# Kernel tuning notes

Hardware: AMD Instinct MI355X
Metric: run time of the kernel (lower is better)

## Reference

```python
import jax, jax.numpy as jnp
import numpy as np
from jax import lax

N = 16384
K = 16
EPS = 1e-5


def setup_inputs() -> dict:
    key = jax.random.key(0)
    ks = jax.random.split(key, 10)

    def w(k, shape):
        fan_in = shape[0]
        return jax.random.normal(k, shape, jnp.float32) / np.sqrt(fan_in)

    return {
        "pos": jax.random.normal(ks[0], (N, 3), jnp.float32),
        "normal": jax.random.normal(ks[1], (N, 3), jnp.float32),
        # conv1 mlp: Linear(9,64) -> GroupNorm(8,64) -> ReLU -> Linear(64,64)
        "W1a": w(ks[2], (9, 64)), "b1a": jnp.zeros((64,), jnp.float32),
        "g1": jnp.ones((64,), jnp.float32), "beta1": jnp.zeros((64,), jnp.float32),
        "W1b": w(ks[3], (64, 64)), "b1b": jnp.zeros((64,), jnp.float32),
        # conv2 mlp: Linear(67,64) -> GroupNorm(8,64) -> ReLU -> Linear(64,64)
        "W2a": w(ks[4], (67, 64)), "b2a": jnp.zeros((64,), jnp.float32),
        "g2": jnp.ones((64,), jnp.float32), "beta2": jnp.zeros((64,), jnp.float32),
        "W2b": w(ks[5], (64, 64)), "b2b": jnp.zeros((64,), jnp.float32),
        # conv3 mlp: Linear(67,128) -> GroupNorm(16,128) -> ReLU -> Linear(128,128)
        "W3a": w(ks[6], (67, 128)), "b3a": jnp.zeros((128,), jnp.float32),
        "g3": jnp.ones((128,), jnp.float32), "beta3": jnp.zeros((128,), jnp.float32),
        "W3b": w(ks[7], (128, 128)), "b3b": jnp.zeros((128,), jnp.float32),
    }


def knn_graph(pos, k):
    # [N,N] squared distances; loop=True -> self is included (distance 0).
    sq = jnp.sum(pos * pos, axis=1)
    d2 = sq[:, None] + sq[None, :] - 2.0 * (pos @ pos.T)
    _, nbr = lax.top_k(-d2, k)  # [N,k] neighbor (source) indices per target node
    return nbr


def group_norm(h, gamma, beta, groups):
    # h: [N,k,C]; normalize each group of channels per edge sample.
    n, k, c = h.shape
    hg = h.reshape(n, k, groups, c // groups)
    mu = hg.mean(axis=-1, keepdims=True)
    var = hg.var(axis=-1, keepdims=True)
    hg = (hg - mu) * lax.rsqrt(var + EPS)
    return hg.reshape(n, k, c) * gamma + beta


def pointnet_conv(x, pos, nbr, Wa, ba, gamma, beta, Wb, bb, groups):
    # message: concat(x_j, pos_j - pos_i), MLP per edge, max-aggregate over neighbors
    xj = x[nbr]                              # [N,k,C_in]
    rel = pos[nbr] - pos[:, None, :]         # [N,k,3]
    m = jnp.concatenate([xj, rel], axis=-1)  # [N,k,C_in+3]
    h = m @ Wa + ba
    h = jax.nn.relu(group_norm(h, gamma, beta, groups))
    h = h @ Wb + bb
    return jnp.max(h, axis=1)                # [N,C_out]


def reference(pos, normal, W1a, b1a, g1, beta1, W1b, b1b,
              W2a, b2a, g2, beta2, W2b, b2b,
              W3a, b3a, g3, beta3, W3b, b3b):
    nbr = knn_graph(pos, K)
    h = jnp.concatenate([pos, normal], axis=-1)  # [N,6]
    h1 = jax.nn.relu(pointnet_conv(h, pos, nbr, W1a, b1a, g1, beta1, W1b, b1b, 8))
    h2 = jax.nn.relu(pointnet_conv(h1, pos, nbr, W2a, b2a, g2, beta2, W2b, b2b, 8))
    h3 = jax.nn.relu(pointnet_conv(h2, pos, nbr, W3a, b3a, g3, beta3, W3b, b3b, 16))
    return (h1, h2, h3)
```

## Files before the change

### kernel.cpp

```cpp
#include <hip/hip_runtime.h>
#include <hip/hip_bf16.h>
#include <stdint.h>

typedef unsigned long long u64;
typedef unsigned int u32;
typedef __attribute__((ext_vector_type(8))) short bf16x8;
typedef __attribute__((ext_vector_type(8))) unsigned short u16x8;
typedef __attribute__((ext_vector_type(4))) float f32x4;

__device__ __forceinline__ float ldv(const void* p, size_t idx, int mode) {
  return mode ? __bfloat162float(((const __hip_bfloat16*)p)[idx])
              : ((const float*)p)[idx];
}
__device__ __forceinline__ void stv(void* p, size_t idx, int mode, float v) {
  if (mode) ((__hip_bfloat16*)p)[idx] = __float2bfloat16(v);
  else      ((float*)p)[idx] = v;
}
__device__ __forceinline__ unsigned short f2bfb(float f) {
  u32 u = __float_as_uint(f);
  u32 r = u + 0x7fffu + ((u >> 16) & 1u);
  return (unsigned short)(r >> 16);
}
__device__ __forceinline__ float bfb2f(unsigned short b) {
  return __uint_as_float((u32)b << 16);
}
__device__ __forceinline__ u64 shfl64(u64 v, int src) {
  int lo = __shfl((int)(u32)(v & 0xffffffffu), src, 64);
  int hi = __shfl((int)(u32)(v >> 32), src, 64);
  return ((u64)(u32)hi << 32) | (u32)lo;
}
__device__ __forceinline__ u64 shflxor64(u64 v, int m) {
  int lo = __shfl_xor((int)(u32)(v & 0xffffffffu), m, 64);
  int hi = __shfl_xor((int)(u32)(v >> 32), m, 64);
  return ((u64)(u32)hi << 32) | (u32)lo;
}
__device__ __forceinline__ u64 shfl64w16(u64 v, int src) {
  int lo = __shfl((int)(u32)(v & 0xffffffffu), src, 16);
  int hi = __shfl((int)(u32)(v >> 32), src, 16);
  return ((u64)(u32)hi << 32) | (u32)lo;
}

__device__ __forceinline__ u32 benc(float f) {
  u32 u = __float_as_uint(f);
  return (u & 0x80000000u) ? ~u : (u | 0x80000000u);
}
__device__ __forceinline__ float bdec(u32 k) {
  return (k & 0x80000000u) ? __uint_as_float(k ^ 0x80000000u)
                           : __uint_as_float(~k);
}

__global__ void PointNetSimple_61409442398998_kernel() {}

struct CvtEnt { const void* src; float* dst; int n; };
struct CvtArgs { CvtEnt e[12]; };
struct WEnt { const void* src; unsigned short* dst; int K, N, Kpad; };
struct WArgs { WEnt e[6]; };

__global__ void setup_kernel(const void* __restrict__ pos,
                             const void* __restrict__ nrm,
                             WArgs wa, CvtArgs ca,
                             int* __restrict__ flag,
                             float4* __restrict__ pos4,
                             float* __restrict__ h0, int n) {
  const unsigned short* u16p = (const unsigned short*)pos;
  int cnt = 0;
  for (int k = 0; k < 32; ++k) {
    int e = (u16p[k] >> 7) & 0xff;
    if (e >= 110 && e <= 140) cnt++;
  }
  const int mode = (cnt >= 26) ? 1 : 0;

  const int nprep = n >> 8;
  const int b = blockIdx.x;
  if (b < nprep) {
    int i = b * 256 + threadIdx.x;
    float x = ldv(pos, 3*(size_t)i+0, mode);
    float y = ldv(pos, 3*(size_t)i+1, mode);
    float z = ldv(pos, 3*(size_t)i+2, mode);
    pos4[i] = make_float4(x, y, z, x*x + y*y + z*z);
    h0[6*(size_t)i+0] = x; h0[6*(size_t)i+1] = y; h0[6*(size_t)i+2] = z;
    h0[6*(size_t)i+3] = ldv(nrm, 3*(size_t)i+0, mode);
    h0[6*(size_t)i+4] = ldv(nrm, 3*(size_t)i+1, mode);
    h0[6*(size_t)i+5] = ldv(nrm, 3*(size_t)i+2, mode);
    float bmn[3] = {x, y, z}, bmx[3] = {x, y, z};
#pragma unroll
    for (int m = 32; m; m >>= 1) {
#pragma unroll
      for (int k = 0; k < 3; ++k) {
        bmn[k] = fminf(bmn[k], __shfl_xor(bmn[k], m, 64));
        bmx[k] = fmaxf(bmx[k], __shfl_xor(bmx[k], m, 64));
      }
    }
    if ((threadIdx.x & 63) == 0) {
      u32* bb = (u32*)flag;
#pragma unroll
      for (int k = 0; k < 3; ++k) {
        atomicMin(&bb[4 + k], benc(bmn[k]));
        atomicMax(&bb[7 + k], benc(bmx[k]));
      }
    }
  } else {
    int r = b - nprep;
    if (r < 6) {
      WEnt ent = wa.e[r];
      for (int t = threadIdx.x; t < ent.N * ent.Kpad; t += blockDim.x) {
        int nn = t / ent.Kpad;
        int k  = t - nn * ent.Kpad;
        float v = (k < ent.K) ? ldv(ent.src, (size_t)k * ent.N + nn, mode) : 0.0f;
        ent.dst[t] = f2bfb(v);
      }
      if (r == 0 && threadIdx.x == 0) flag[0] = mode;
    } else {
      for (int t2 = 0; t2 < 12; ++t2) {
        CvtEnt ent = ca.e[t2];
        for (int t = threadIdx.x; t < ent.n; t += blockDim.x)
          ent.dst[t] = ldv(ent.src, t, mode);
      }
    }
  }
}

template<int CAP>
__device__ __forceinline__ void knn_flush(u64* __restrict__ wbuf, int& cnt,
                                          u64& val, u64& t15, float& th,
                                          int lane) {
  u64 cand = (lane < cnt) ? wbuf[lane] : ~0ull;
#pragma unroll
  for (int k = 2; k <= CAP; k <<= 1) {
#pragma unroll
    for (int j = k >> 1; j > 0; j >>= 1) {
      u64 other = shflxor64(cand, j);
      bool up    = ((lane & k) == 0) || (k == CAP);
      bool lower = ((lane & j) == 0);
      bool keepMin = (up == lower);
      u64 mn = cand < other ? cand : other;
      u64 mx = cand < other ? other : cand;
      cand = keepMin ? mn : mx;
    }
  }
  u64 rev = shfl64w16(cand, 15 - (lane & 15));
  u64 lo = val < rev ? val : rev;
#pragma unroll
  for (int j = 8; j > 0; j >>= 1) {
    u64 other = shflxor64(lo, j);
    bool lower = ((lane & j) == 0);
    u64 mn = lo < other ? lo : other;
    u64 mx = lo < other ? other : lo;
    lo = lower ? mn : mx;
  }
  val = (lane < 16) ? lo : ~0ull;
  t15 = shfl64(val, 15);
  u32 thb = (u32)(t15 >> 32);
  th = (thb == 0xffffffffu) ? 3.4e38f : __uint_as_float(thb);
  cnt = 0;
}

#define GR 32
#define GR3 (GR*GR*GR)

__global__ __launch_bounds__(256) void hist_kernel(
    const float4* __restrict__ pos4, const u32* __restrict__ bbx,
    int* __restrict__ counts, int* __restrict__ cid, int n) {
  const int i = blockIdx.x * 256 + threadIdx.x;
  if (i >= n) return;
  const float mnx = bdec(bbx[0]), mny = bdec(bbx[1]), mnz = bdec(bbx[2]);
  const float ihx = (float)GR / fmaxf(bdec(bbx[3]) - mnx, 1e-20f);
  const float ihy = (float)GR / fmaxf(bdec(bbx[4]) - mny, 1e-20f);
  const float ihz = (float)GR / fmaxf(bdec(bbx[5]) - mnz, 1e-20f);
  float4 p = pos4[i];
  int cx = min(GR - 1, max(0, (int)((p.x - mnx) * ihx)));
  int cy = min(GR - 1, max(0, (int)((p.y - mny) * ihy)));
  int cz = min(GR - 1, max(0, (int)((p.z - mnz) * ihz)));
  int lin = (cz * GR + cy) * GR + cx;
  cid[i] = lin;
  atomicAdd(&counts[lin], 1);
}

__global__ __launch_bounds__(1024) void scan_kernel(
    const int* __restrict__ counts, int* __restrict__ cellstart,
    int* __restrict__ cursor) {
  __shared__ int part[1024];
  const int t = threadIdx.x;
  const int base = t * 32;
  int v[32];
  int s = 0;
#pragma unroll
  for (int k = 0; k < 32; ++k) { v[k] = counts[base + k]; s += v[k]; }
  part[t] = s;
  __syncthreads();
  for (int d = 1; d < 1024; d <<= 1) {
    int x = (t >= d) ? part[t - d] : 0;
    __syncthreads();
    part[t] += x;
    __syncthreads();
  }
  int off = part[t] - s;
#pragma unroll
  for (int k = 0; k < 32; ++k) {
    cellstart[base + k] = off; cursor[base + k] = off; off += v[k];
  }
  if (t == 1023) { cellstart[GR3] = off; cursor[GR3] = off; }
}

__global__ __launch_bounds__(256) void scatter_kernel(
    const float4* __restrict__ pos4, const int* __restrict__ cid,
    int* __restrict__ cursor, int* __restrict__ sidx,
    float4* __restrict__ spos4, int n) {
  const int i = blockIdx.x * 256 + threadIdx.x;
  if (i >= n) return;
  int dst = atomicAdd(&cursor[cid[i]], 1);
  spos4[dst] = pos4[i];
  sidx[dst]  = i;
}

#define KNN7_WPB 4
__global__ __launch_bounds__(256) void knn7_kernel(
    const float4* __restrict__ spos4,
    const int* __restrict__ sidx, const int* __restrict__ cellstart,
    const u32* __restrict__ bbx, int* __restrict__ nbr, int n) {
  __shared__ u64 buf[KNN7_WPB][72];
  const int tid = threadIdx.x, lane = tid & 63, w = tid >> 6;
  const int g = blockIdx.x * KNN7_WPB + w;
  u64* wbuf = &buf[w][0];
  const float4 pi = spos4[g];
  const int target = sidx[g];

  const float mnx = bdec(bbx[0]), mny = bdec(bbx[1]), mnz = bdec(bbx[2]);
  const float ex = fmaxf(bdec(bbx[3]) - mnx, 1e-20f);
  const float ey = fmaxf(bdec(bbx[4]) - mny, 1e-20f);
  const float ez = fmaxf(bdec(bbx[5]) - mnz, 1e-20f);
  const float ihx = (float)GR / ex, ihy = (float)GR / ey, ihz = (float)GR / ez;
  const float hxf = ex * (1.0f / GR), hyf = ey * (1.0f / GR), hzf = ez * (1.0f / GR);
  const int cx = min(GR - 1, max(0, (int)((pi.x - mnx) * ihx)));
  const int cy = min(GR - 1, max(0, (int)((pi.y - mny) * ihy)));
  const int cz = min(GR - 1, max(0, (int)((pi.z - mnz) * ihz)));

  u64 val = ~0ull, t15 = ~0ull;
  float th = 3.4e38f;
  int cnt = 0;
  int myseen = 0;

  auto doFlush = [&]() {
    if (cnt <= 32) knn_flush<32>(wbuf, cnt, val, t15, th, lane);
    else           knn_flush<64>(wbuf, cnt, val, t15, th, lane);
  };

  auto procSeg = [&](int p0, int p1) {
#pragma unroll 2
    for (int t0 = p0; t0 < p1; t0 += 64) {
      int gi = t0 + lane;
      bool in = gi < p1;
      float4 a = spos4[in ? gi : (p1 - 1)];
      float d2 = (pi.w + a.w) - 2.0f*(pi.x*a.x + pi.y*a.y + pi.z*a.z);
      d2 = fmaxf(d2, 0.0f);
      bool pass = in && (d2 <= th);
      u64 bal = __ballot(pass);
      if (bal) {
        int pc = __popcll(bal);
        if (cnt + pc > 64) doFlush();
        u32 mb = __builtin_amdgcn_mbcnt_lo((u32)bal, 0u);
        mb = __builtin_amdgcn_mbcnt_hi((u32)(bal >> 32), mb);
        if (pass)
          wbuf[cnt + mb] = ((u64)__float_as_uint(d2) << 32) | (u32)sidx[gi];
        cnt += pc;
      }
    }
  };

  {
    const int oc = (cz * GR + cy) * GR + cx;
    const int oLo = cellstart[oc], oHi = cellstart[oc + 1];
    if (lane == 0) myseen += oHi - oLo;
    procSeg(oLo, oHi);
    if (cnt > 0) doFlush();
  }

  for (int r = 1; r < GR; ++r) {
    const int x0 = max(cx - r, 0), x1 = min(cx + r, GR - 1);
    const int d1 = 2*r + 1, d2i = 2*r - 1;
    const int nA = 2 * d1;
    const int nB = 2 * d2i;
    const int nC = 2 * d2i * d2i;
    const int S = nA + nB + nC;
    const u32 magic = 0xFFFFFFFFu / (u32)d2i + 1u;

    for (int b0 = 0; b0 < S; b0 += 64) {
      const int s = b0 + lane;
      int zc = 0, yc = 0, xa = 0, xb = -1;
      bool live = s < S;
      if (live) {
        if (s < nA) {
          int za = s >= d1;
          int dy = s - (za ? d1 : 0) - r;
          zc = cz + (za ? r : -r); yc = cy + dy; xa = x0; xb = x1;
        } else if (s < nA + nB) {
          int t = s - nA;
          int side = t >= d2i;
          int dz = t - (side ? d2i : 0) - (r - 1);
          zc = cz + dz; yc = cy + (side ? r : -r); xa = x0; xb = x1;
        } else {
          int t = s - nA - nB;
          int side = t & 1; t >>= 1;
          int dzi = (int)__umulhi((u32)t, magic);
          int dyi = t - dzi * d2i;
          zc = cz - r + 1 + dzi; yc = cy - r + 1 + dyi;
          int xcell = side ? cx + r : cx - r;
          xa = xcell; xb = xcell;
          live = ((unsigned)xcell < GR);
        }
        live = live && ((unsigned)zc < GR) && ((unsigned)yc < GR);
      }
      int lo = 0, hi = 0;
      if (live) {
        int base = (zc * GR + yc) * GR;
        lo = cellstart[base + xa];
        hi = cellstart[base + xb + 1];
        myseen += hi - lo;
      }
      u64 bal = __ballot(live && (hi > lo));
      while (bal) {
        int l = __builtin_ctzll(bal); bal &= bal - 1;
        int p0 = __shfl(lo, l, 64), p1 = __shfl(hi, l, 64);
        procSeg(p0, p1);
      }
    }

    int tot = myseen;
#pragma unroll
    for (int m = 32; m; m >>= 1) tot += __shfl_xor(tot, m, 64);
    if (tot >= n) break;
    float mind = 3.4e38f;
    if (cx - r > 0)      mind = fminf(mind, pi.x - (mnx + (float)(cx - r) * hxf));
    if (cx + r < GR - 1) mind = fminf(mind, (mnx + (float)(cx + r + 1) * hxf) - pi.x);
    if (cy - r > 0)      mind = fminf(mind, pi.y - (mny + (float)(cy - r) * hyf));
    if (cy + r < GR - 1) mind = fminf(mind, (mny + (float)(cy + r + 1) * hyf) - pi.y);
    if (cz - r > 0)      mind = fminf(mind, pi.z - (mnz + (float)(cz - r) * hzf));
    if (cz + r < GR - 1) mind = fminf(mind, (mnz + (float)(cz + r + 1) * hzf) - pi.z);
    float mind2 = mind * mind * 0.9999f - 1e-6f;
    if (mind2 > th) break;
    if (cnt > 0) {
      doFlush();
      if (mind2 > th) break;
    }
  }
  if (cnt > 0) doFlush();
  if (lane < 16) nbr[(size_t)target * 16 + lane] = (int)(val & 0xffffffffu);
}

template<int CIN, int CMID, int KT1, int NT, int KT2>
__global__ __launch_bounds__(256, 4) void conv_mfma7_kernel(
    const float* __restrict__ xf,
    const unsigned short* __restrict__ xb,
    const float4* __restrict__ pos4,
    const int* __restrict__ nbr,
    const int* __restrict__ flag,
    const unsigned short* __restrict__ WaT,
    const unsigned short* __restrict__ WbT,
    const float* __restrict__ baf,
    const float* __restrict__ gmf,
    const float* __restrict__ btf,
    const float* __restrict__ bbf,
    unsigned short* __restrict__ xoutb,
    void* __restrict__ bout, size_t out_off)
{
  constexpr int K1PAD = KT1 * 32;
  constexpr int SB = CMID + 8;

  __shared__ unsigned short msgB[128 * SB];

  const int tid  = threadIdx.x;
  const int lane = tid & 63;
  const int w    = tid >> 6;
  const int quad = lane >> 4;
  const int cl   = lane & 15;
  const int node0 = blockIdx.x * 8;
  const int mode = flag[0];

  bf16x8 afr[2][KT1];
#pragma unroll
  for (int mt = 0; mt < 2; ++mt) {
    const int node = node0 + w*2 + mt;
    const int j = nbr[(size_t)node*16 + cl];
    const float4 pin = pos4[node];
    const float4 pj = pos4[j];
    const float rx = pj.x - pin.x, ry = pj.y - pin.y, rz = pj.z - pin.z;
    if constexpr (CIN == 64) {
#pragma unroll
      for (int kt = 0; kt < 2; ++kt)
        afr[mt][kt] = *(const bf16x8*)&xb[(size_t)j*64 + kt*32 + quad*8];
      unsigned short o[8] = {0,0,0,0,0,0,0,0};
      if (quad == 0) { o[0] = f2bfb(rx); o[1] = f2bfb(ry); o[2] = f2bfb(rz); }
      afr[mt][KT1-1] = *(bf16x8*)o;
    } else {
      unsigned short o[8] = {0,0,0,0,0,0,0,0};
      if (quad == 0) {
        const float* p = &xf[(size_t)j*6];
        o[0] = f2bfb(p[0]); o[1] = f2bfb(p[1]); o[2] = f2bfb(p[2]);
        o[3] = f2bfb(p[3]); o[4] = f2bfb(p[4]); o[5] = f2bfb(p[5]);
        o[6] = f2bfb(rx);   o[7] = f2bfb(ry);
      } else if (quad == 1) {
        o[0] = f2bfb(rz);
      }
      afr[mt][0] = *(bf16x8*)o;
    }
  }

  const int grow = lane >> 1, ggl = lane & 1;
  bf16x8 w1c[KT1], w1n[KT1];
#pragma unroll
  for (int kt = 0; kt < KT1; ++kt)
    w1c[kt] = *(const bf16x8*)&WaT[(size_t)cl * K1PAD + kt*32 + quad*8];
#pragma unroll
  for (int nt = 0; nt < NT; ++nt) {
    if (nt + 1 < NT) {
#pragma unroll
      for (int kt = 0; kt < KT1; ++kt)
        w1n[kt] = *(const bf16x8*)&WaT[(size_t)((nt+1)*16 + cl) * K1PAD + kt*32 + quad*8];
    }
    f32x4 a1[2];
    a1[0] = (f32x4){0.f, 0.f, 0.f, 0.f};
    a1[1] = (f32x4){0.f, 0.f, 0.f, 0.f};
#pragma unroll
    for (int kt = 0; kt < KT1; ++kt) {
      a1[0] = __builtin_amdgcn_mfma_f32_16x16x32_bf16(afr[0][kt], w1c[kt], a1[0], 0, 0, 0);
      a1[1] = __builtin_amdgcn_mfma_f32_16x16x32_bf16(afr[1][kt], w1c[kt], a1[1], 0, 0, 0);
    }
    float bac = baf[nt*16 + cl];
#pragma unroll
    for (int mt = 0; mt < 2; ++mt)
#pragma unroll
      for (int reg = 0; reg < 4; ++reg)
        msgB[(w*32 + mt*16 + quad*4 + reg) * SB + nt*16 + cl] =
            f2bfb(a1[mt][reg] + bac);
    asm volatile("" ::: "memory");
    {
      const int cb = nt*16 + ggl*8;
      unsigned short* p = &msgB[(w*32 + grow) * SB + cb];
      u16x8 hv = *(const u16x8*)p;
      float vv[8];
#pragma unroll
      for (int e = 0; e < 8; ++e) vv[e] = bfb2f(hv[e]);
      float s = 0.f, q = 0.f;
#pragma unroll
      for (int e = 0; e < 8; ++e) { s += vv[e]; q += vv[e]*vv[e]; }
      float mu = s * 0.125f;
      float var = q * 0.125f - mu * mu;
      float inv = rsqrtf(fmaxf(var, 0.0f) + 1e-5f);
      unsigned short o[8];
#pragma unroll
      for (int e = 0; e < 8; ++e) {
        float t = (vv[e] - mu) * inv * gmf[cb+e] + btf[cb+e];
        o[e] = f2bfb(fmaxf(t, 0.0f));
      }
      *(bf16x8*)p = *(bf16x8*)o;
    }
    asm volatile("" ::: "memory");
#pragma unroll
    for (int kt = 0; kt < KT1; ++kt) w1c[kt] = w1n[kt];
  }

  bf16x8 af0[KT2], af1[KT2];
#pragma unroll
  for (int kt = 0; kt < KT2; ++kt) {
    af0[kt] = *(const bf16x8*)&msgB[(w*32 + cl)      * SB + kt*32 + quad*8];
    af1[kt] = *(const bf16x8*)&msgB[(w*32 + 16 + cl) * SB + kt*32 + quad*8];
  }
  bf16x8 w2c[KT2], w2n[KT2];
#pragma unroll
  for (int kt = 0; kt < KT2; ++kt)
    w2c[kt] = *(const bf16x8*)&WbT[(size_t)cl * CMID + kt*32 + quad*8];
#pragma unroll
  for (int nt = 0; nt < NT; ++nt) {
    if (nt + 1 < NT) {
#pragma unroll
      for (int kt = 0; kt < KT2; ++kt)
        w2n[kt] = *(const bf16x8*)&WbT[(size_t)((nt+1)*16 + cl) * CMID + kt*32 + quad*8];
    }
    f32x4 a2[2];
    a2[0] = (f32x4){0.f, 0.f, 0.f, 0.f};
    a2[1] = (f32x4){0.f, 0.f, 0.f, 0.f};
#pragma unroll
    for (int kt = 0; kt < KT2; ++kt) {
      a2[0] = __builtin_amdgcn_mfma_f32_16x16x32_bf16(af0[kt], w2c[kt], a2[0], 0, 0, 0);
      a2[1] = __builtin_amdgcn_mfma_f32_16x16x32_bf16(af1[kt], w2c[kt], a2[1], 0, 0, 0);
    }
#pragma unroll
    for (int mt = 0; mt < 2; ++mt) {
      int node = node0 + w*2 + mt;
      float m = fmaxf(fmaxf(a2[mt][0], a2[mt][1]),
                      fmaxf(a2[mt][2], a2[mt][3]));
      m = fmaxf(m, __shfl_xor(m, 16, 64));
      m = fmaxf(m, __shfl_xor(m, 32, 64));
      float v = fmaxf(m + bbf[nt*16 + cl], 0.0f);
      if (quad == 0) {
        size_t oi = (size_t)node * CMID + nt*16 + cl;
        if (xoutb) xoutb[oi] = f2bfb(v);
        stv(bout, out_off + oi, mode, v);
      }
    }
#pragma unroll
    for (int kt = 0; kt < KT2; ++kt) w2c[kt] = w2n[kt];
  }
}

extern "C" void kernel_launch(void* const* d_in, const int* in_sizes, int n_in,
                              void* d_out, int out_size, void* d_ws, size_t ws_size,
                              hipStream_t stream) {
  (void)n_in; (void)ws_size; (void)in_sizes;
  int n = out_size / 256;
  if (n <= 0 || (n & 255)) n = 16384;

  float* ws = (float*)d_ws;
  int*    flag    = (int*)ws;
  float4* pos4    = (float4*)(ws + 16);
  float*  h0      = ws + 16 + (size_t)4*n;
  int*    nbr     = (int*)(ws + 16 + (size_t)10*n);
  unsigned short* h1b = (unsigned short*)(ws + 16 + (size_t)26*n);
  unsigned short* h2b = (unsigned short*)(ws + 16 + (size_t)58*n);
  float*  vbuf    = ws + 16 + (size_t)90*n;
  unsigned short* wtbuf = (unsigned short*)(vbuf + 1024);

  float* gbase = vbuf + 1024 + 22528;
  int*    cid       = (int*)gbase;
  int*    counts    = cid + n;
  int*    cellstart = counts + GR3;
  int*    cursor    = cellstart + 32772;
  int*    sidx      = cursor + 32772;
  float4* spos4     = (float4*)(sidx + n);

  const int vsz[12] = {64,64,64,64, 64,64,64,64, 128,128,128,128};
  const int vsrc[12] = {3,4,5,7, 9,10,11,13, 15,16,17,19};
  CvtArgs ca;
  float* vptr[12];
  {
    int off = 0;
    for (int t = 0; t < 12; ++t) {
      ca.e[t].src = d_in[vsrc[t]];
      ca.e[t].dst = vbuf + off;
      ca.e[t].n   = vsz[t];
      vptr[t] = vbuf + off;
      off += vsz[t];
    }
  }
  const int wK[6]    = {9, 64, 67, 64, 67, 128};
  const int wN[6]    = {64, 64, 64, 64, 128, 128};
  const int wKp[6]   = {32, 64, 96, 64, 96, 128};
  const int wsrc[6]  = {2, 6, 8, 12, 14, 18};
  WArgs wa;
  unsigned short* wptr[6];
  {
    int off = 0;
    for (int t = 0; t < 6; ++t) {
      wa.e[t].src  = d_in[wsrc[t]];
      wa.e[t].dst  = wtbuf + off;
      wa.e[t].K    = wK[t];
      wa.e[t].N    = wN[t];
      wa.e[t].Kpad = wKp[t];
      wptr[t] = wtbuf + off;
      off += wN[t] * wKp[t];
    }
  }

  u32* bbx = (u32*)ws + 4;
  hipMemsetAsync(bbx,     0xFF, 12, stream);
  hipMemsetAsync(bbx + 3, 0x00, 12, stream);
  hipMemsetAsync(counts,  0x00, GR3 * sizeof(int), stream);

  setup_kernel<<<n/256 + 7, 256, 0, stream>>>(
      d_in[0], d_in[1], wa, ca, flag, pos4, h0, n);

  hist_kernel<<<n/256, 256, 0, stream>>>(pos4, bbx, counts, cid, n);
  scan_kernel<<<1, 1024, 0, stream>>>(counts, cellstart, cursor);
  scatter_kernel<<<n/256, 256, 0, stream>>>(pos4, cid, cursor, sidx, spos4, n);
  knn7_kernel<<<n/KNN7_WPB, 256, 0, stream>>>(spos4, sidx, cellstart,
                                              bbx, nbr, n);

  conv_mfma7_kernel<6, 64, 1, 4, 2><<<n/8, 256, 0, stream>>>(
      h0, (const unsigned short*)nullptr, pos4, nbr, flag, wptr[0], wptr[1],
      vptr[0], vptr[1], vptr[2], vptr[3], h1b, d_out, (size_t)0);
  conv_mfma7_kernel<64, 64, 3, 4, 2><<<n/8, 256, 0, stream>>>(
      (const float*)nullptr, h1b, pos4, nbr, flag, wptr[2], wptr[3],
      vptr[4], vptr[5], vptr[6], vptr[7], h2b, d_out, (size_t)n*64);
  conv_mfma7_kernel<64, 128, 3, 8, 4><<<n/8, 256, 0, stream>>>(
      (const float*)nullptr, h2b, pos4, nbr, flag, wptr[4], wptr[5],
      vptr[8], vptr[9], vptr[10], vptr[11],
      (unsigned short*)nullptr, d_out, (size_t)n*128);
}
```

Measured before the change: 351.6 us.

## Fold memsets into setup kernel and make kNN a persistent work-stealing kernel

Removes two of the three memsets: the bbox max is now encoded as a negated min, so a single 0xFF memset covers all six words, and the cell-count zeroing moves into extra setup_kernel blocks. The scan kernel now uses int4 vector loads and stores, and resets counts[0] so it can be reused as an atomic work counter. The kNN kernel becomes persistent: 1024 blocks whose wavefronts take query points from that atomic counter, which balances the uneven per-point search cost. This adds an atomic per query and depends on counts[0] being zeroed before the kNN launch.

```diff
diff --git a/kernel.cpp b/kernel.cpp
--- a/kernel.cpp
+++ b/kernel.cpp
@@ -56,12 +56,16 @@
 struct WEnt { const void* src; unsigned short* dst; int K, N, Kpad; };
 struct WArgs { WEnt e[6]; };
 
+#define GR 32
+#define GR3 (GR*GR*GR)
+
 __global__ void setup_kernel(const void* __restrict__ pos,
                              const void* __restrict__ nrm,
                              WArgs wa, CvtArgs ca,
                              int* __restrict__ flag,
                              float4* __restrict__ pos4,
-                             float* __restrict__ h0, int n) {
+                             float* __restrict__ h0,
+                             int* __restrict__ counts, int n) {
   const unsigned short* u16p = (const unsigned short*)pos;
   int cnt = 0;
   for (int k = 0; k < 32; ++k) {
@@ -96,7 +100,7 @@
 #pragma unroll
       for (int k = 0; k < 3; ++k) {
         atomicMin(&bb[4 + k], benc(bmn[k]));
-        atomicMax(&bb[7 + k], benc(bmx[k]));
+        atomicMin(&bb[7 + k], benc(-bmx[k]));
       }
     }
   } else {
@@ -110,12 +114,14 @@
         ent.dst[t] = f2bfb(v);
       }
       if (r == 0 && threadIdx.x == 0) flag[0] = mode;
-    } else {
+    } else if (r == 6) {
       for (int t2 = 0; t2 < 12; ++t2) {
         CvtEnt ent = ca.e[t2];
         for (int t = threadIdx.x; t < ent.n; t += blockDim.x)
           ent.dst[t] = ldv(ent.src, t, mode);
       }
+    } else {
+      counts[(r - 7) * 256 + threadIdx.x] = 0;
     }
   }
 }
@@ -155,18 +161,15 @@
   cnt = 0;
 }
 
-#define GR 32
-#define GR3 (GR*GR*GR)
-
 __global__ __launch_bounds__(256) void hist_kernel(
     const float4* __restrict__ pos4, const u32* __restrict__ bbx,
     int* __restrict__ counts, int* __restrict__ cid, int n) {
   const int i = blockIdx.x * 256 + threadIdx.x;
   if (i >= n) return;
   const float mnx = bdec(bbx[0]), mny = bdec(bbx[1]), mnz = bdec(bbx[2]);
-  const float ihx = (float)GR / fmaxf(bdec(bbx[3]) - mnx, 1e-20f);
-  const float ihy = (float)GR / fmaxf(bdec(bbx[4]) - mny, 1e-20f);
-  const float ihz = (float)GR / fmaxf(bdec(bbx[5]) - mnz, 1e-20f);
+  const float ihx = (float)GR / fmaxf(-bdec(bbx[3]) - mnx, 1e-20f);
+  const float ihy = (float)GR / fmaxf(-bdec(bbx[4]) - mny, 1e-20f);
+  const float ihz = (float)GR / fmaxf(-bdec(bbx[5]) - mnz, 1e-20f);
   float4 p = pos4[i];
   int cx = min(GR - 1, max(0, (int)((p.x - mnx) * ihx)));
   int cy = min(GR - 1, max(0, (int)((p.y - mny) * ihy)));
@@ -181,25 +184,34 @@
     int* __restrict__ cursor) {
   __shared__ int part[1024];
   const int t = threadIdx.x;
-  const int base = t * 32;
-  int v[32];
+  int4 v[8];
   int s = 0;
 #pragma unroll
-  for (int k = 0; k < 32; ++k) { v[k] = counts[base + k]; s += v[k]; }
+  for (int k = 0; k < 8; ++k) {
+    v[k] = ((const int4*)counts)[t*8 + k];
+    s += v[k].x + v[k].y + v[k].z + v[k].w;
+  }
   part[t] = s;
   __syncthreads();
+  if (t == 0) ((int*)counts)[0] = 0;
   for (int d = 1; d < 1024; d <<= 1) {
     int x = (t >= d) ? part[t - d] : 0;
     __syncthreads();
     part[t] += x;
     __syncthreads();
   }
-  int off = part[t] - s;
-#pragma unroll
-  for (int k = 0; k < 32; ++k) {
-    cellstart[base + k] = off; cursor[base + k] = off; off += v[k];
-  }
-  if (t == 1023) { cellstart[GR3] = off; cursor[GR3] = off; }
+  int o = part[t] - s;
+#pragma unroll
+  for (int k = 0; k < 8; ++k) {
+    int4 c;
+    c.x = o; o += v[k].x;
+    c.y = o; o += v[k].y;
+    c.z = o; o += v[k].z;
+    c.w = o; o += v[k].w;
+    ((int4*)cellstart)[t*8 + k] = c;
+    ((int4*)cursor)[t*8 + k] = c;
+  }
+  if (t == 1023) { cellstart[GR3] = o; cursor[GR3] = o; }
 }
 
 __global__ __launch_bounds__(256) void scatter_kernel(
@@ -213,138 +225,146 @@
   sidx[dst]  = i;
 }
 
-#define KNN7_WPB 4
-__global__ __launch_bounds__(256) void knn7_kernel(
+#define KNN_BLOCKS 1024
+__global__ __launch_bounds__(256) void knn7p_kernel(
     const float4* __restrict__ spos4,
     const int* __restrict__ sidx, const int* __restrict__ cellstart,
-    const u32* __restrict__ bbx, int* __restrict__ nbr, int n) {
-  __shared__ u64 buf[KNN7_WPB][72];
+    const u32* __restrict__ bbx, int* __restrict__ nbr,
+    int* __restrict__ ctr, int n) {
+  __shared__ u64 buf[4][72];
   const int tid = threadIdx.x, lane = tid & 63, w = tid >> 6;
-  const int g = blockIdx.x * KNN7_WPB + w;
   u64* wbuf = &buf[w][0];
-  const float4 pi = spos4[g];
-  const int target = sidx[g];
 
   const float mnx = bdec(bbx[0]), mny = bdec(bbx[1]), mnz = bdec(bbx[2]);
-  const float ex = fmaxf(bdec(bbx[3]) - mnx, 1e-20f);
-  const float ey = fmaxf(bdec(bbx[4]) - mny, 1e-20f);
-  const float ez = fmaxf(bdec(bbx[5]) - mnz, 1e-20f);
+  const float ex = fmaxf(-bdec(bbx[3]) - mnx, 1e-20f);
+  const float ey = fmaxf(-bdec(bbx[4]) - mny, 1e-20f);
+  const float ez = fmaxf(-bdec(bbx[5]) - mnz, 1e-20f);
   const float ihx = (float)GR / ex, ihy = (float)GR / ey, ihz = (float)GR / ez;
   const float hxf = ex * (1.0f / GR), hyf = ey * (1.0f / GR), hzf = ez * (1.0f / GR);
-  const int cx = min(GR - 1, max(0, (int)((pi.x - mnx) * ihx)));
-  const int cy = min(GR - 1, max(0, (int)((pi.y - mny) * ihy)));
-  const int cz = min(GR - 1, max(0, (int)((pi.z - mnz) * ihz)));
-
-  u64 val = ~0ull, t15 = ~0ull;
-  float th = 3.4e38f;
-  int cnt = 0;
-  int myseen = 0;
-
-  auto doFlush = [&]() {
-    if (cnt <= 32) knn_flush<32>(wbuf, cnt, val, t15, th, lane);
-    else           knn_flush<64>(wbuf, cnt, val, t15, th, lane);
-  };
-
-  auto procSeg = [&](int p0, int p1) {
+
+  for (;;) {
+    int g0 = 0;
+    if (lane == 0) g0 = atomicAdd(ctr, 1);
+    const int g = __shfl(g0, 0, 64);
+    if (g >= n) break;
+
+    const float4 pi = spos4[g];
+    const int target = sidx[g];
+    const int cx = min(GR - 1, max(0, (int)((pi.x - mnx) * ihx)));
+    const int cy = min(GR - 1, max(0, (int)((pi.y - mny) * ihy)));
+    const int cz = min(GR - 1, max(0, (int)((pi.z - mnz) * ihz)));
+
+    u64 val = ~0ull, t15 = ~0ull;
+    float th = 3.4e38f;
+    int cnt = 0;
+    int myseen = 0;
+
+    auto doFlush = [&]() {
+      if (cnt <= 32) knn_flush<32>(wbuf, cnt, val, t15, th, lane);
+      else           knn_flush<64>(wbuf, cnt, val, t15, th, lane);
+    };
+
+    auto procSeg = [&](int p0, int p1) {
 #pragma unroll 2
-    for (int t0 = p0; t0 < p1; t0 += 64) {
-      int gi = t0 + lane;
-      bool in = gi < p1;
-      float4 a = spos4[in ? gi : (p1 - 1)];
-      float d2 = (pi.w + a.w) - 2.0f*(pi.x*a.x + pi.y*a.y + pi.z*a.z);
-      d2 = fmaxf(d2, 0.0f);
-      bool pass = in && (d2 <= th);
-      u64 bal = __ballot(pass);
-      if (bal) {
-        int pc = __popcll(bal);
-        if (cnt + pc > 64) doFlush();
-        u32 mb = __builtin_amdgcn_mbcnt_lo((u32)bal, 0u);
-        mb = __builtin_amdgcn_mbcnt_hi((u32)(bal >> 32), mb);
-        if (pass)
-          wbuf[cnt + mb] = ((u64)__float_as_uint(d2) << 32) | (u32)sidx[gi];
-        cnt += pc;
-      }
-    }
-  };
-
-  {
-    const int oc = (cz * GR + cy) * GR + cx;
-    const int oLo = cellstart[oc], oHi = cellstart[oc + 1];
-    if (lane == 0) myseen += oHi - oLo;
-    procSeg(oLo, oHi);
+      for (int t0 = p0; t0 < p1; t0 += 64) {
+        int gi = t0 + lane;
+        bool in = gi < p1;
+        float4 a = spos4[in ? gi : (p1 - 1)];
+        float d2 = (pi.w + a.w) - 2.0f*(pi.x*a.x + pi.y*a.y + pi.z*a.z);
+        d2 = fmaxf(d2, 0.0f);
+        bool pass = in && (d2 <= th);
+        u64 bal = __ballot(pass);
+        if (bal) {
+          int pc = __popcll(bal);
+          if (cnt + pc > 64) doFlush();
+          u32 mb = __builtin_amdgcn_mbcnt_lo((u32)bal, 0u);
+          mb = __builtin_amdgcn_mbcnt_hi((u32)(bal >> 32), mb);
+          if (pass)
+            wbuf[cnt + mb] = ((u64)__float_as_uint(d2) << 32) | (u32)sidx[gi];
+          cnt += pc;
+        }
+      }
+    };
+
+    {
+      const int oc = (cz * GR + cy) * GR + cx;
+      const int oLo = cellstart[oc], oHi = cellstart[oc + 1];
+      if (lane == 0) myseen += oHi - oLo;
+      procSeg(oLo, oHi);
+      if (cnt > 0) doFlush();
+    }
+
+    for (int r = 1; r < GR; ++r) {
+      const int x0 = max(cx - r, 0), x1 = min(cx + r, GR - 1);
+      const int d1 = 2*r + 1, d2i = 2*r - 1;
+      const int nA = 2 * d1;
+      const int nB = 2 * d2i;
+      const int nC = 2 * d2i * d2i;
+      const int S = nA + nB + nC;
+      const u32 magic = 0xFFFFFFFFu / (u32)d2i + 1u;
+
+      for (int b0 = 0; b0 < S; b0 += 64) {
+        const int s = b0 + lane;
+        int zc = 0, yc = 0, xa = 0, xb = -1;
+        bool live = s < S;
+        if (live) {
+          if (s < nA) {
+            int za = s >= d1;
+            int dy = s - (za ? d1 : 0) - r;
+            zc = cz + (za ? r : -r); yc = cy + dy; xa = x0; xb = x1;
+          } else if (s < nA + nB) {
+            int t = s - nA;
+            int side = t >= d2i;
+            int dz = t - (side ? d2i : 0) - (r - 1);
+            zc = cz + dz; yc = cy + (side ? r : -r); xa = x0; xb = x1;
+          } else {
+            int t = s - nA - nB;
+            int side = t & 1; t >>= 1;
+            int dzi = (int)__umulhi((u32)t, magic);
+            int dyi = t - dzi * d2i;
+            zc = cz - r + 1 + dzi; yc = cy - r + 1 + dyi;
+            int xcell = side ? cx + r : cx - r;
+            xa = xcell; xb = xcell;
+            live = ((unsigned)xcell < GR);
+          }
+          live = live && ((unsigned)zc < GR) && ((unsigned)yc < GR);
+        }
+        int lo = 0, hi = 0;
+        if (live) {
+          int base = (zc * GR + yc) * GR;
+          lo = cellstart[base + xa];
+          hi = cellstart[base + xb + 1];
+          myseen += hi - lo;
+        }
+        u64 bal = __ballot(live && (hi > lo));
+        while (bal) {
+          int l = __builtin_ctzll(bal); bal &= bal - 1;
+          int p0 = __shfl(lo, l, 64), p1 = __shfl(hi, l, 64);
+          procSeg(p0, p1);
+        }
+      }
+
+      int tot = myseen;
+#pragma unroll
+      for (int m = 32; m; m >>= 1) tot += __shfl_xor(tot, m, 64);
+      if (tot >= n) break;
+      float mind = 3.4e38f;
+      if (cx - r > 0)      mind = fminf(mind, pi.x - (mnx + (float)(cx - r) * hxf));
+      if (cx + r < GR - 1) mind = fminf(mind, (mnx + (float)(cx + r + 1) * hxf) - pi.x);
+      if (cy - r > 0)      mind = fminf(mind, pi.y - (mny + (float)(cy - r) * hyf));
+      if (cy + r < GR - 1) mind = fminf(mind, (mny + (float)(cy + r + 1) * hyf) - pi.y);
+      if (cz - r > 0)      mind = fminf(mind, pi.z - (mnz + (float)(cz - r) * hzf));
+      if (cz + r < GR - 1) mind = fminf(mind, (mnz + (float)(cz + r + 1) * hzf) - pi.z);
+      float mind2 = mind * mind * 0.9999f - 1e-6f;
+      if (mind2 > th) break;
+      if (cnt > 0) {
+        doFlush();
+        if (mind2 > th) break;
+      }
+    }
     if (cnt > 0) doFlush();
-  }
-
-  for (int r = 1; r < GR; ++r) {
-    const int x0 = max(cx - r, 0), x1 = min(cx + r, GR - 1);
-    const int d1 = 2*r + 1, d2i = 2*r - 1;
-    const int nA = 2 * d1;
-    const int nB = 2 * d2i;
-    const int nC = 2 * d2i * d2i;
-    const int S = nA + nB + nC;
-    const u32 magic = 0xFFFFFFFFu / (u32)d2i + 1u;
-
-    for (int b0 = 0; b0 < S; b0 += 64) {
-      const int s = b0 + lane;
-      int zc = 0, yc = 0, xa = 0, xb = -1;
-      bool live = s < S;
-      if (live) {
-        if (s < nA) {
-          int za = s >= d1;
-          int dy = s - (za ? d1 : 0) - r;
-          zc = cz + (za ? r : -r); yc = cy + dy; xa = x0; xb = x1;
-        } else if (s < nA + nB) {
-          int t = s - nA;
-          int side = t >= d2i;
-          int dz = t - (side ? d2i : 0) - (r - 1);
-          zc = cz + dz; yc = cy + (side ? r : -r); xa = x0; xb = x1;
-        } else {
-          int t = s - nA - nB;
-          int side = t & 1; t >>= 1;
-          int dzi = (int)__umulhi((u32)t, magic);
-          int dyi = t - dzi * d2i;
-          zc = cz - r + 1 + dzi; yc = cy - r + 1 + dyi;
-          int xcell = side ? cx + r : cx - r;
-          xa = xcell; xb = xcell;
-          live = ((unsigned)xcell < GR);
-        }
-        live = live && ((unsigned)zc < GR) && ((unsigned)yc < GR);
-      }
-      int lo = 0, hi = 0;
-      if (live) {
-        int base = (zc * GR + yc) * GR;
-        lo = cellstart[base + xa];
-        hi = cellstart[base + xb + 1];
-        myseen += hi - lo;
-      }
-      u64 bal = __ballot(live && (hi > lo));
-      while (bal) {
-        int l = __builtin_ctzll(bal); bal &= bal - 1;
-        int p0 = __shfl(lo, l, 64), p1 = __shfl(hi, l, 64);
-        procSeg(p0, p1);
-      }
-    }
-
-    int tot = myseen;
-#pragma unroll
-    for (int m = 32; m; m >>= 1) tot += __shfl_xor(tot, m, 64);
-    if (tot >= n) break;
-    float mind = 3.4e38f;
-    if (cx - r > 0)      mind = fminf(mind, pi.x - (mnx + (float)(cx - r) * hxf));
-    if (cx + r < GR - 1) mind = fminf(mind, (mnx + (float)(cx + r + 1) * hxf) - pi.x);
-    if (cy - r > 0)      mind = fminf(mind, pi.y - (mny + (float)(cy - r) * hyf));
-    if (cy + r < GR - 1) mind = fminf(mind, (mny + (float)(cy + r + 1) * hyf) - pi.y);
-    if (cz - r > 0)      mind = fminf(mind, pi.z - (mnz + (float)(cz - r) * hzf));
-    if (cz + r < GR - 1) mind = fminf(mind, (mnz + (float)(cz + r + 1) * hzf) - pi.z);
-    float mind2 = mind * mind * 0.9999f - 1e-6f;
-    if (mind2 > th) break;
-    if (cnt > 0) {
-      doFlush();
-      if (mind2 > th) break;
-    }
-  }
-  if (cnt > 0) doFlush();
-  if (lane < 16) nbr[(size_t)target * 16 + lane] = (int)(val & 0xffffffffu);
+    if (lane < 16) nbr[(size_t)target * 16 + lane] = (int)(val & 0xffffffffu);
+  }
 }
 
 template<int CIN, int CMID, int KT1, int NT, int KT2>
@@ -562,18 +582,16 @@
   }
 
   u32* bbx = (u32*)ws + 4;
-  hipMemsetAsync(bbx,     0xFF, 12, stream);
-  hipMemsetAsync(bbx + 3, 0x00, 12, stream);
-  hipMemsetAsync(counts,  0x00, GR3 * sizeof(int), stream);
-
-  setup_kernel<<<n/256 + 7, 256, 0, stream>>>(
-      d_in[0], d_in[1], wa, ca, flag, pos4, h0, n);
+  hipMemsetAsync(bbx, 0xFF, 24, stream);
+
+  setup_kernel<<<n/256 + 7 + GR3/256, 256, 0, stream>>>(
+      d_in[0], d_in[1], wa, ca, flag, pos4, h0, counts, n);
 
   hist_kernel<<<n/256, 256, 0, stream>>>(pos4, bbx, counts, cid, n);
   scan_kernel<<<1, 1024, 0, stream>>>(counts, cellstart, cursor);
   scatter_kernel<<<n/256, 256, 0, stream>>>(pos4, cid, cursor, sidx, spos4, n);
-  knn7_kernel<<<n/KNN7_WPB, 256, 0, stream>>>(spos4, sidx, cellstart,
-                                              bbx, nbr, n);
+  knn7p_kernel<<<KNN_BLOCKS, 256, 0, stream>>>(spos4, sidx, cellstart,
+                                               bbx, nbr, counts, n);
 
   conv_mfma7_kernel<6, 64, 1, 4, 2><<<n/8, 256, 0, stream>>>(
       h0, (const unsigned short*)nullptr, pos4, nbr, flag, wptr[0], wptr[1],
```

Measured after the change: 524.4 us. +49.1%, slower.
